# Optimization experiments

Hardware: AMD Instinct MI355X
Metric: run time of the kernel (lower is better)

Reference implementation:

```python
import jax, jax.numpy as jnp
import numpy as np

B, S, D = 4, 2048, 512
H = 8
DK = D // H
DFF = 2048
EPS = 1e-5


def _layernorm(x, g, b):
    mu = jnp.mean(x, axis=-1, keepdims=True)
    var = jnp.mean((x - mu) ** 2, axis=-1, keepdims=True)
    return (x - mu) * jax.lax.rsqrt(var + EPS) * g + b


def setup_inputs() -> dict:
    key = jax.random.key(0)
    ks = jax.random.split(key, 12)
    s = 1.0 / np.sqrt(D)
    sf = 1.0 / np.sqrt(DFF)
    return {
        "x": jax.random.normal(ks[0], (B, S, D), dtype=jnp.float32),
        "Wq": jax.random.uniform(ks[1], (D, D), jnp.float32, -s, s),
        "bq": jnp.zeros((D,), jnp.float32),
        "Wk": jax.random.uniform(ks[2], (D, D), jnp.float32, -s, s),
        "bk": jnp.zeros((D,), jnp.float32),
        "Wv": jax.random.uniform(ks[3], (D, D), jnp.float32, -s, s),
        "bv": jnp.zeros((D,), jnp.float32),
        "Wo": jax.random.uniform(ks[4], (D, D), jnp.float32, -s, s),
        "bo": jnp.zeros((D,), jnp.float32),
        "W1": jax.random.uniform(ks[5], (D, DFF), jnp.float32, -s, s),
        "b1": jnp.zeros((DFF,), jnp.float32),
        "W2": jax.random.uniform(ks[6], (DFF, D), jnp.float32, -sf, sf),
        "b2": jnp.zeros((D,), jnp.float32),
        "g1": jnp.ones((D,), jnp.float32),
        "be1": jnp.zeros((D,), jnp.float32),
        "g2": jnp.ones((D,), jnp.float32),
        "be2": jnp.zeros((D,), jnp.float32),
    }


def reference(x, Wq, bq, Wk, bk, Wv, bv, Wo, bo, W1, b1, W2, b2, g1, be1, g2, be2):
    # Multi-head attention (dropout = identity at eval)
    def heads(v):  # [B,S,D] -> [B,H,S,DK]
        return v.reshape(B, S, H, DK).transpose(0, 2, 1, 3)

    q = heads(x @ Wq + bq)
    k = heads(x @ Wk + bk)
    v = heads(x @ Wv + bv)
    scores = jnp.einsum("bhsd,bhtd->bhst", q, k) / np.sqrt(DK)
    attn = jax.nn.softmax(scores, axis=-1)
    ctx = jnp.einsum("bhst,bhtd->bhsd", attn, v)
    ctx = ctx.transpose(0, 2, 1, 3).reshape(B, S, D)
    attn_out = ctx @ Wo + bo

    x1 = _layernorm(x + attn_out, g1, be1)

    ff = jax.nn.relu(x1 @ W1 + b1) @ W2 + b2
    return _layernorm(x1 + ff, g2, be2)
```

## Files before the change

kernel.cpp:

```cpp
#include <hip/hip_runtime.h>
#include <hip/hip_bf16.h>
#include <stdint.h>

typedef __bf16 bf16;
typedef __attribute__((ext_vector_type(8))) __bf16 bf16x8;
typedef __attribute__((ext_vector_type(4))) float f32x4;

#define DEVI __device__ __forceinline__

constexpr int Bz = 4, Sz = 2048, Dz = 512, Hz = 8, DKz = 64, DFFz = 2048;
constexpr int ROWSz = Bz * Sz;
constexpr float EPSf = 1e-5f;
constexpr float C2f = 0.125f * 1.44269504088896f;

DEVI void load_lds16(void* lds, const void* g) {
  __builtin_amdgcn_global_load_lds(
      (const __attribute__((address_space(1))) void*)(uintptr_t)(g),
      (__attribute__((address_space(3))) void*)(uint32_t)(uintptr_t)(lds),
      16, 0, 0);
}

DEVI void permswap32(unsigned& x, unsigned& y) {
  asm("v_permlane32_swap_b32 %0, %1" : "+v"(x), "+v"(y));
}
DEVI void permswap16(unsigned& x, unsigned& y) {
  asm("v_permlane16_swap_b32 %0, %1" : "+v"(x), "+v"(y));
}

template <int BM, int BK, int EPI>
__global__ __launch_bounds__(256, BM == 128 ? 4 : 3) void gemm_bt(
    const bf16* __restrict__ A, const bf16* __restrict__ Bt,
    const float* __restrict__ bias, const float* __restrict__ resid,
    const bf16* __restrict__ residb, bf16* __restrict__ aux,
    void* __restrict__ Cout, int M, int N, int K) {
  constexpr int BN = 128;
  constexpr int MI = BM / 32;
  constexpr int RPI = 512 / BK;
  constexpr int AISS = (BM / 4) / RPI;
  constexpr int BISS = 32 / RPI;
  __shared__ alignas(16) bf16 sA[2][BM * BK];
  __shared__ alignas(16) bf16 sB[2][BN * BK];
  const int tid = threadIdx.x;
  const int lane = tid & 63;
  const int wv = tid >> 6;
  const int n0 = blockIdx.x * BN;
  const int m0 = blockIdx.y * BM;

  const int srow = (BK == 32) ? (lane >> 2) : (lane >> 3);
  const int sch = (BK == 32) ? (((lane & 3) ^ (srow & 3)) * 8)
                             : (((lane & 7) ^ (srow & 7)) * 8);
  const bf16* gA = A + (size_t)(m0 + wv * (BM / 4) + srow) * K + sch;
  const bf16* gB = Bt + (size_t)(n0 + wv * 32 + srow) * K + sch;

  const int wm = (wv >> 1) * (BM / 2);
  const int wn = (wv & 1) * 64;
  const int fr = lane & 15;
  const int fq = lane >> 4;

  auto stage = [&](int buf, int k0) {
#pragma unroll
    for (int j = 0; j < AISS; ++j)
      load_lds16(sA[buf] + (wv * (BM / 4) + j * RPI) * BK, gA + (size_t)(j * RPI) * K + k0);
#pragma unroll
    for (int j = 0; j < BISS; ++j)
      load_lds16(sB[buf] + (wv * 32 + j * RPI) * BK, gB + (size_t)(j * RPI) * K + k0);
  };

  f32x4 acc[MI][4] = {};

  stage(0, 0);
  __syncthreads();

  const int niter = K / BK;
  for (int it = 0; it < niter; ++it) {
    const int cur = it & 1;
    if (it + 1 < niter) stage(cur ^ 1, (it + 1) * BK);
#pragma unroll
    for (int kk = 0; kk < BK / 32; ++kk) {
      const int fc = (BK == 32) ? ((fq ^ (fr & 3)) * 8)
                                : (((4 * kk + fq) ^ (fr & 7)) * 8);
      bf16x8 af[MI], bfr[4];
#pragma unroll
      for (int i = 0; i < MI; ++i)
        af[i] = *(const bf16x8*)(sA[cur] + (wm + i * 16 + fr) * BK + fc);
#pragma unroll
      for (int j = 0; j < 4; ++j)
        bfr[j] = *(const bf16x8*)(sB[cur] + (wn + j * 16 + fr) * BK + fc);
#pragma unroll
      for (int i = 0; i < MI; ++i)
#pragma unroll
        for (int j = 0; j < 4; ++j)
          acc[i][j] = __builtin_amdgcn_mfma_f32_16x16x32_bf16(af[i], bfr[j], acc[i][j], 0, 0, 0);
    }
    __syncthreads();
  }

#pragma unroll
  for (int i = 0; i < MI; ++i) {
#pragma unroll
    for (int j = 0; j < 4; ++j) {
      const int col = n0 + wn + j * 16 + fr;
      const float bv = bias[col];
      if (EPI == 3 && col >= 1024) {
        const int row0 = m0 + wm + i * 16 + fq * 4;
        const int hh = (col - 1024) >> 6, dk = (col - 1024) & 63;
        const int bb = row0 >> 11, s0 = row0 & 2047;
        bf16 pv[4];
#pragma unroll
        for (int r = 0; r < 4; ++r) pv[r] = (bf16)(acc[i][j][r] + bv);
        *(uint2*)(aux + (size_t)((bb * 8 + hh) * 64 + dk) * 2048 + s0) = *(const uint2*)pv;
      } else {
#pragma unroll
        for (int r = 0; r < 4; ++r) {
          const int row = m0 + wm + i * 16 + fq * 4 + r;
          const size_t idx = (size_t)row * N + col;
          float v = acc[i][j][r] + bv;
          if (EPI == 1) {
            ((bf16*)Cout)[idx] = (bf16)(v + resid[idx]);
          } else if (EPI == 2) {
            ((bf16*)Cout)[idx] = (bf16)(v > 0.f ? v : 0.f);
          } else if (EPI == 3) {
            ((bf16*)Cout)[idx] = (bf16)(col < 512 ? v * C2f : v);
          } else {
            ((bf16*)Cout)[idx] = (bf16)(v + (float)residb[idx]);
          }
        }
      }
    }
  }
}

__global__ __launch_bounds__(256, 4) void flash_attn(
    const bf16* __restrict__ qkv, const bf16* __restrict__ Vt,
    bf16* __restrict__ ctx) {
  const int bid = blockIdx.x;
  const int qt = bid >> 5;
  const int bh = bid & 31;
  const int h = bh & 7;
  const int b = bh >> 3;
  const int q0 = qt * 64;
  const int tid = threadIdx.x, lane = tid & 63, wv = tid >> 6;
  const int fr = lane & 15, fq = lane >> 4;
  const int xsw = fr & 7;

  __shared__ alignas(16) bf16 sK[2][64 * 64];
  __shared__ alignas(16) bf16 sV[2][64 * 64];

  const int srow = lane >> 3;
  const int scol = ((lane & 7) ^ srow) * 8;

  const bf16* gQ = qkv + (size_t)(b * Sz + q0 + wv * 16 + srow) * 1536 + h * 64 + scol;
  const bf16* gK = qkv + (size_t)(b * Sz + wv * 16 + srow) * 1536 + 512 + h * 64 + scol;
  const bf16* gV = Vt + (size_t)((b * 8 + h) * 64 + wv * 16 + srow) * Sz + scol;

  auto stage = [&](int buf, int t) {
    const size_t t0r = (size_t)t * 64;
    load_lds16(sK[buf] + (wv * 16 + 0) * 64, gK + t0r * 1536);
    load_lds16(sK[buf] + (wv * 16 + 8) * 64, gK + (t0r + 8) * 1536);
    load_lds16(sV[buf] + (wv * 16 + 0) * 64, gV + t0r);
    load_lds16(sV[buf] + (wv * 16 + 8) * 64, gV + (size_t)8 * Sz + t0r);
  };

  bf16* sQ = (bf16*)sV[1];
  load_lds16(sQ + (wv * 16 + 0) * 64, gQ);
  load_lds16(sQ + (wv * 16 + 8) * 64, gQ + (size_t)8 * 1536);
  stage(0, 0);
  asm volatile("s_waitcnt vmcnt(4)" ::: "memory");

  const int colc0 = (fq ^ xsw) * 8;
  const int colc1 = ((fq + 4) ^ xsw) * 8;
  int qsrc[4];
#pragma unroll
  for (int r = 0; r < 4; ++r) qsrc[r] = (fq * 4 + r) | (lane & 48);

  bf16x8 qb[2];
  qb[0] = *(const bf16x8*)(sQ + (wv * 16 + fr) * 64 + colc0);
  qb[1] = *(const bf16x8*)(sQ + (wv * 16 + fr) * 64 + colc1);
  asm volatile("s_waitcnt lgkmcnt(0)" ::: "memory");
  stage(1, 1);
  asm volatile("s_waitcnt vmcnt(4)" ::: "memory");
  __builtin_amdgcn_s_barrier();
  asm volatile("" ::: "memory");

  float l_part = 0.f;
  f32x4 acc_o[4] = {};

  for (int t = 0; t < 32; ++t) {
    const int cur = t & 1;
    if (t >= 1 && t + 1 < 32) stage(cur ^ 1, t + 1);

    bf16x8 kf[2][4];
#pragma unroll
    for (int j = 0; j < 4; ++j) {
      kf[0][j] = *(const bf16x8*)(sK[cur] + (j * 16 + fr) * 64 + colc0);
      kf[1][j] = *(const bf16x8*)(sK[cur] + (j * 16 + fr) * 64 + colc1);
    }
    f32x4 sc[4];
    __builtin_amdgcn_s_setprio(1);
#pragma unroll
    for (int j = 0; j < 4; ++j) {
      f32x4 z = {0.f, 0.f, 0.f, 0.f};
      z = __builtin_amdgcn_mfma_f32_16x16x32_bf16(kf[0][j], qb[0], z, 0, 0, 0);
      sc[j] = __builtin_amdgcn_mfma_f32_16x16x32_bf16(kf[1][j], qb[1], z, 0, 0, 0);
    }
    __builtin_amdgcn_s_setprio(0);

    unsigned c0[4], c1[4];
    float rs = 0.f;
#pragma unroll
    for (int j = 0; j < 4; ++j) {
      float e0 = __builtin_amdgcn_exp2f(sc[j][0]);
      float e1 = __builtin_amdgcn_exp2f(sc[j][1]);
      float e2 = __builtin_amdgcn_exp2f(sc[j][2]);
      float e3 = __builtin_amdgcn_exp2f(sc[j][3]);
      rs += (e0 + e1) + (e2 + e3);
      union { bf16 hh[2]; unsigned u; } pka, pkb;
      pka.hh[0] = (bf16)e0; pka.hh[1] = (bf16)e1;
      pkb.hh[0] = (bf16)e2; pkb.hh[1] = (bf16)e3;
      c0[j] = pka.u;
      c1[j] = pkb.u;
    }
    l_part += rs;

    bf16x8 pa[2];
#pragma unroll
    for (int kk = 0; kk < 2; ++kk) {
      unsigned x0 = c0[2 * kk], y0 = c0[2 * kk + 1];
      permswap32(x0, y0);
      permswap16(x0, y0);
      unsigned x1 = c1[2 * kk], y1 = c1[2 * kk + 1];
      permswap32(x1, y1);
      permswap16(x1, y1);
      union { unsigned u[4]; bf16x8 v; } pk;
      pk.u[0] = x0; pk.u[1] = x1; pk.u[2] = y0; pk.u[3] = y1;
      pa[kk] = pk.v;
    }

    bf16x8 vf[2][4];
#pragma unroll
    for (int j = 0; j < 4; ++j) {
      vf[0][j] = *(const bf16x8*)(sV[cur] + (j * 16 + fr) * 64 + colc0);
      vf[1][j] = *(const bf16x8*)(sV[cur] + (j * 16 + fr) * 64 + colc1);
    }
    __builtin_amdgcn_s_setprio(1);
#pragma unroll
    for (int kk = 0; kk < 2; ++kk)
#pragma unroll
      for (int j = 0; j < 4; ++j)
        acc_o[j] = __builtin_amdgcn_mfma_f32_16x16x32_bf16(pa[kk], vf[kk][j], acc_o[j], 0, 0, 0);
    __builtin_amdgcn_s_setprio(0);

    if (t + 1 < 32) {
      asm volatile("s_waitcnt vmcnt(0)" ::: "memory");
      __builtin_amdgcn_s_barrier();
      asm volatile("" ::: "memory");
    }
  }

  float l = l_part;
  l += __shfl_xor(l, 16, 64);
  l += __shfl_xor(l, 32, 64);
  float rl[4];
#pragma unroll
  for (int r = 0; r < 4; ++r) rl[r] = 1.0f / __shfl(l, qsrc[r], 64);
#pragma unroll
  for (int j = 0; j < 4; ++j)
#pragma unroll
    for (int r = 0; r < 4; ++r) {
      const int row = b * Sz + q0 + wv * 16 + fq * 4 + r;
      const int col = h * 64 + j * 16 + fr;
      ctx[(size_t)row * Dz + col] = (bf16)(acc_o[j][r] * rl[r]);
    }
}

template <int OUT_F32>
__global__ __launch_bounds__(256) void layer_norm_k(
    const bf16* __restrict__ y, const float* __restrict__ g,
    const float* __restrict__ be, void* __restrict__ out) {
  const int row = blockIdx.x * 4 + (threadIdx.x >> 6);
  const int lane = threadIdx.x & 63;
  const int col = lane * 8;
  bf16x8 hv = *(const bf16x8*)(y + (size_t)row * Dz + col);
  float v[8];
  float s = 0.f, ss = 0.f;
#pragma unroll
  for (int i = 0; i < 8; ++i) {
    v[i] = (float)hv[i];
    s += v[i];
    ss += v[i] * v[i];
  }
#pragma unroll
  for (int o = 1; o < 64; o <<= 1) {
    s += __shfl_xor(s, o, 64);
    ss += __shfl_xor(ss, o, 64);
  }
  const float mu = s * (1.0f / Dz);
  const float rstd = rsqrtf(ss * (1.0f / Dz) - mu * mu + EPSf);
  const float4* g4 = (const float4*)(g + col);
  const float4* b4 = (const float4*)(be + col);
  float4 ga = g4[0], gb = g4[1], ba = b4[0], bb = b4[1];
  float o8[8];
  o8[0] = (v[0] - mu) * rstd * ga.x + ba.x;
  o8[1] = (v[1] - mu) * rstd * ga.y + ba.y;
  o8[2] = (v[2] - mu) * rstd * ga.z + ba.z;
  o8[3] = (v[3] - mu) * rstd * ga.w + ba.w;
  o8[4] = (v[4] - mu) * rstd * gb.x + bb.x;
  o8[5] = (v[5] - mu) * rstd * gb.y + bb.y;
  o8[6] = (v[6] - mu) * rstd * gb.z + bb.z;
  o8[7] = (v[7] - mu) * rstd * gb.w + bb.w;
  if (OUT_F32) {
    float4* of = (float4*)((float*)out + (size_t)row * Dz + col);
    of[0] = make_float4(o8[0], o8[1], o8[2], o8[3]);
    of[1] = make_float4(o8[4], o8[5], o8[6], o8[7]);
  } else {
    bf16 ob[8];
#pragma unroll
    for (int i = 0; i < 8; ++i) ob[i] = (bf16)o8[i];
    *(uint4*)((bf16*)out + (size_t)row * Dz + col) = *(const uint4*)ob;
  }
}

__global__ __launch_bounds__(256) void prep_all(
    const float* __restrict__ Wq, const float* __restrict__ Wk,
    const float* __restrict__ Wv, const float* __restrict__ Wo,
    const float* __restrict__ W1, const float* __restrict__ W2,
    const float* __restrict__ bq, const float* __restrict__ bk,
    const float* __restrict__ bv, const float* __restrict__ x,
    bf16* __restrict__ WqkvT, bf16* __restrict__ WoT,
    bf16* __restrict__ W1T, bf16* __restrict__ W2T,
    float* __restrict__ bqkv, bf16* __restrict__ xb) {
  __shared__ float tile[64][65];
  const int blk = blockIdx.x;
  const int t = threadIdx.x;
  if (blk < 768) {
    const float* W;
    bf16* Wt;
    int K, N, local;
    if (blk < 64)       { W = Wq; Wt = WqkvT;                       K = 512;  N = 512;  local = blk; }
    else if (blk < 128) { W = Wk; Wt = WqkvT + (size_t)512 * 512;   K = 512;  N = 512;  local = blk - 64; }
    else if (blk < 192) { W = Wv; Wt = WqkvT + (size_t)1024 * 512;  K = 512;  N = 512;  local = blk - 128; }
    else if (blk < 256) { W = Wo; Wt = WoT;                         K = 512;  N = 512;  local = blk - 192; }
    else if (blk < 512) { W = W1; Wt = W1T;                         K = 512;  N = 2048; local = blk - 256; }
    else                { W = W2; Wt = W2T;                         K = 2048; N = 512;  local = blk - 512; }
    const int kt = K / 64;
    const int k0 = (local % kt) * 64, n0 = (local / kt) * 64;
    const int r = t >> 2, c = (t & 3) * 16;
    const float* src = W + (size_t)(k0 + r) * N + n0 + c;
#pragma unroll
    for (int i = 0; i < 4; ++i) {
      float4 v = ((const float4*)src)[i];
      tile[r][c + i * 4 + 0] = v.x;
      tile[r][c + i * 4 + 1] = v.y;
      tile[r][c + i * 4 + 2] = v.z;
      tile[r][c + i * 4 + 3] = v.w;
    }
    __syncthreads();
    union { bf16 hh[16]; uint4 u[2]; } pk;
#pragma unroll
    for (int i = 0; i < 16; ++i) pk.hh[i] = (bf16)tile[c + i][r];
    uint4* dst = (uint4*)(Wt + (size_t)(n0 + r) * K + k0 + c);
    dst[0] = pk.u[0];
    dst[1] = pk.u[1];
  } else if (blk == 768) {
    for (int i = t; i < 1536; i += 256)
      bqkv[i] = i < 512 ? bq[i] : (i < 1024 ? bk[i - 512] : bv[i - 1024]);
  } else {
    const int local = blk - 769;
#pragma unroll
    for (int k = 0; k < 4; ++k) {
      const int i = local * 1024 + k * 256 + t;
      float4 v = ((const float4*)x)[i];
      bf16 tv[4] = {(bf16)v.x, (bf16)v.y, (bf16)v.z, (bf16)v.w};
      ((uint2*)xb)[i] = *(const uint2*)tv;
    }
  }
}

extern "C" void kernel_launch(void* const* d_in, const int* in_sizes, int n_in,
                              void* d_out, int out_size, void* d_ws, size_t ws_size,
                              hipStream_t stream) {
  const float* x   = (const float*)d_in[0];
  const float* Wq  = (const float*)d_in[1];
  const float* bq  = (const float*)d_in[2];
  const float* Wk  = (const float*)d_in[3];
  const float* bk  = (const float*)d_in[4];
  const float* Wv  = (const float*)d_in[5];
  const float* bvp = (const float*)d_in[6];
  const float* Wo  = (const float*)d_in[7];
  const float* bo  = (const float*)d_in[8];
  const float* W1  = (const float*)d_in[9];
  const float* b1  = (const float*)d_in[10];
  const float* W2  = (const float*)d_in[11];
  const float* b2  = (const float*)d_in[12];
  const float* g1  = (const float*)d_in[13];
  const float* be1 = (const float*)d_in[14];
  const float* g2  = (const float*)d_in[15];
  const float* be2 = (const float*)d_in[16];

  char* ws = (char*)d_ws;
  size_t off = 0;
  auto alloc = [&](size_t bytes) -> void* {
    void* p = ws + off;
    off += (bytes + 255) & ~(size_t)255;
    return p;
  };
  bf16*  WqkvT = (bf16*)alloc((size_t)1536 * 512 * 2);
  float* bqkv  = (float*)alloc(1536 * 4);
  bf16*  WoT   = (bf16*)alloc((size_t)512 * 512 * 2);
  bf16*  W1T   = (bf16*)alloc((size_t)2048 * 512 * 2);
  bf16*  W2T   = (bf16*)alloc((size_t)512 * 2048 * 2);
  bf16*  xb    = (bf16*)alloc((size_t)ROWSz * 512 * 2);
  bf16*  qkv   = (bf16*)alloc((size_t)ROWSz * 1536 * 2);
  bf16*  Vt    = (bf16*)alloc((size_t)32 * 64 * 2048 * 2);
  bf16*  ctx   = (bf16*)alloc((size_t)ROWSz * 512 * 2);
  bf16*  y1    = (bf16*)alloc((size_t)ROWSz * 512 * 2);
  bf16*  x1b   = (bf16*)alloc((size_t)ROWSz * 512 * 2);
  bf16*  hbuf  = qkv;
  bf16*  y2    = y1;

  prep_all<<<dim3(1793), 256, 0, stream>>>(Wq, Wk, Wv, Wo, W1, W2, bq, bk, bvp, x,
                                           WqkvT, WoT, W1T, W2T, bqkv, xb);

  gemm_bt<128, 32, 3><<<dim3(12, 64), 256, 0, stream>>>(xb, WqkvT, bqkv, nullptr, nullptr, Vt, qkv, ROWSz, 1536, 512);
  flash_attn<<<dim3(1024), 256, 0, stream>>>(qkv, Vt, ctx);
  gemm_bt<64, 64, 4><<<dim3(4, 128), 256, 0, stream>>>(ctx, WoT, bo, nullptr, xb, nullptr, y1, ROWSz, 512, 512);
  layer_norm_k<0><<<dim3(2048), 256, 0, stream>>>(y1, g1, be1, x1b);
  gemm_bt<128, 32, 2><<<dim3(16, 64), 256, 0, stream>>>(x1b, W1T, b1, nullptr, nullptr, nullptr, hbuf, ROWSz, 2048, 512);
  gemm_bt<64, 64, 4><<<dim3(4, 128), 256, 0, stream>>>(hbuf, W2T, b2, nullptr, x1b, nullptr, y2, ROWSz, 512, 2048);
  layer_norm_k<1><<<dim3(2048), 256, 0, stream>>>(y2, g2, be2, d_out);
}
```

Measured before the change: 245.8 us.

## Use 8-wave flash-attention blocks with triple-buffered K/V and direct Q loads

The attention kernel now runs 512-thread blocks covering 128 query rows each, so every K/V tile staged in LDS is shared by twice as many waves. Staging moves from double to triple buffering with a two-tile prefetch distance, waiting only on the oldest load before each barrier. Q fragments are now read straight from global memory into registers instead of passing through LDS. The goal is to halve K/V global traffic per query and hide load latency better. The cost is more LDS per block, fewer blocks (512) to spread across CUs, and barriers that span eight waves.

```diff
diff --git a/kernel.cpp b/kernel.cpp
--- a/kernel.cpp
+++ b/kernel.cpp
@@ -130,7 +130,7 @@
   }
 }
 
-__global__ __launch_bounds__(256, 4) void flash_attn(
+__global__ __launch_bounds__(512, 4) void flash_attn(
     const bf16* __restrict__ qkv, const bf16* __restrict__ Vt,
     bf16* __restrict__ ctx) {
   const int bid = blockIdx.x;
@@ -138,34 +138,37 @@
   const int bh = bid & 31;
   const int h = bh & 7;
   const int b = bh >> 3;
-  const int q0 = qt * 64;
+  const int q0 = qt * 128;
   const int tid = threadIdx.x, lane = tid & 63, wv = tid >> 6;
   const int fr = lane & 15, fq = lane >> 4;
   const int xsw = fr & 7;
 
-  __shared__ alignas(16) bf16 sK[2][64 * 64];
-  __shared__ alignas(16) bf16 sV[2][64 * 64];
+  __shared__ alignas(16) bf16 sK[3][64 * 64];
+  __shared__ alignas(16) bf16 sV[3][64 * 64];
 
   const int srow = lane >> 3;
   const int scol = ((lane & 7) ^ srow) * 8;
 
-  const bf16* gQ = qkv + (size_t)(b * Sz + q0 + wv * 16 + srow) * 1536 + h * 64 + scol;
-  const bf16* gK = qkv + (size_t)(b * Sz + wv * 16 + srow) * 1536 + 512 + h * 64 + scol;
-  const bf16* gV = Vt + (size_t)((b * 8 + h) * 64 + wv * 16 + srow) * Sz + scol;
+  const bf16* gK = qkv + (size_t)(b * Sz + wv * 8 + srow) * 1536 + 512 + h * 64 + scol;
+  const bf16* gV = Vt + (size_t)((b * 8 + h) * 64 + wv * 8 + srow) * Sz + scol;
 
   auto stage = [&](int buf, int t) {
-    const size_t t0r = (size_t)t * 64;
-    load_lds16(sK[buf] + (wv * 16 + 0) * 64, gK + t0r * 1536);
-    load_lds16(sK[buf] + (wv * 16 + 8) * 64, gK + (t0r + 8) * 1536);
-    load_lds16(sV[buf] + (wv * 16 + 0) * 64, gV + t0r);
-    load_lds16(sV[buf] + (wv * 16 + 8) * 64, gV + (size_t)8 * Sz + t0r);
+    const size_t t0 = (size_t)t * 64;
+    load_lds16(sK[buf] + (wv * 8) * 64, gK + t0 * 1536);
+    load_lds16(sV[buf] + (wv * 8) * 64, gV + t0);
   };
 
-  bf16* sQ = (bf16*)sV[1];
-  load_lds16(sQ + (wv * 16 + 0) * 64, gQ);
-  load_lds16(sQ + (wv * 16 + 8) * 64, gQ + (size_t)8 * 1536);
+  const bf16* gQf = qkv + (size_t)(b * Sz + q0 + wv * 16 + fr) * 1536 + h * 64;
+  bf16x8 qb[2];
+  qb[0] = *(const bf16x8*)(gQf + fq * 8);
+  qb[1] = *(const bf16x8*)(gQf + (fq + 4) * 8);
+
   stage(0, 0);
-  asm volatile("s_waitcnt vmcnt(4)" ::: "memory");
+  stage(1, 1);
+  stage(2, 2);
+  asm volatile("s_waitcnt vmcnt(2)" ::: "memory");
+  __builtin_amdgcn_s_barrier();
+  asm volatile("" ::: "memory");
 
   const int colc0 = (fq ^ xsw) * 8;
   const int colc1 = ((fq + 4) ^ xsw) * 8;
@@ -173,21 +176,16 @@
 #pragma unroll
   for (int r = 0; r < 4; ++r) qsrc[r] = (fq * 4 + r) | (lane & 48);
 
-  bf16x8 qb[2];
-  qb[0] = *(const bf16x8*)(sQ + (wv * 16 + fr) * 64 + colc0);
-  qb[1] = *(const bf16x8*)(sQ + (wv * 16 + fr) * 64 + colc1);
-  asm volatile("s_waitcnt lgkmcnt(0)" ::: "memory");
-  stage(1, 1);
-  asm volatile("s_waitcnt vmcnt(4)" ::: "memory");
-  __builtin_amdgcn_s_barrier();
-  asm volatile("" ::: "memory");
-
   float l_part = 0.f;
   f32x4 acc_o[4] = {};
+  int cur = 0;
 
   for (int t = 0; t < 32; ++t) {
-    const int cur = t & 1;
-    if (t >= 1 && t + 1 < 32) stage(cur ^ 1, t + 1);
+    if (t >= 1 && t + 2 < 32) {
+      int nb = cur + 2;
+      if (nb >= 3) nb -= 3;
+      stage(nb, t + 2);
+    }
 
     bf16x8 kf[2][4];
 #pragma unroll
@@ -250,11 +248,13 @@
         acc_o[j] = __builtin_amdgcn_mfma_f32_16x16x32_bf16(pa[kk], vf[kk][j], acc_o[j], 0, 0, 0);
     __builtin_amdgcn_s_setprio(0);
 
-    if (t + 1 < 32) {
-      asm volatile("s_waitcnt vmcnt(0)" ::: "memory");
+    if (t < 31) {
+      if (t <= 29) asm volatile("s_waitcnt vmcnt(2)" ::: "memory");
+      else         asm volatile("s_waitcnt vmcnt(0)" ::: "memory");
       __builtin_amdgcn_s_barrier();
       asm volatile("" ::: "memory");
     }
+    cur = cur == 2 ? 0 : cur + 1;
   }
 
   float l = l_part;
@@ -422,7 +422,7 @@
                                            WqkvT, WoT, W1T, W2T, bqkv, xb);
 
   gemm_bt<128, 32, 3><<<dim3(12, 64), 256, 0, stream>>>(xb, WqkvT, bqkv, nullptr, nullptr, Vt, qkv, ROWSz, 1536, 512);
-  flash_attn<<<dim3(1024), 256, 0, stream>>>(qkv, Vt, ctx);
+  flash_attn<<<dim3(512), 512, 0, stream>>>(qkv, Vt, ctx);
   gemm_bt<64, 64, 4><<<dim3(4, 128), 256, 0, stream>>>(ctx, WoT, bo, nullptr, xb, nullptr, y1, ROWSz, 512, 512);
   layer_norm_k<0><<<dim3(2048), 256, 0, stream>>>(y1, g1, be1, x1b);
   gemm_bt<128, 32, 2><<<dim3(16, 64), 256, 0, stream>>>(x1b, W1T, b1, nullptr, nullptr, nullptr, hbuf, ROWSz, 2048, 512);
```

Measured after the change: 244.4 us. Within noise of the previous version (-0.6%).
